# Kernel optimization log

Measured on AMD Instinct MI355X. Metric: run time of the kernel, lower is better.

Reference implementation:

```python
import jax, jax.numpy as jnp
import numpy as np

N_PTS = 2_000_000
N_VOX = 500_000
N_EMB = 1_000_000
EMBED_DIM = 16


def _interp_offset():
    # 8 corners of the unit cube, same order as torch.meshgrid([0,1]*3) -> reshape(-1,3)
    o = jnp.array([0.0, 1.0], dtype=jnp.float32)
    return jnp.stack(jnp.meshgrid(o, o, o, indexing='ij'), axis=-1).reshape(-1, 3)  # [8,3]


def setup_inputs() -> dict:
    key = jax.random.key(0)
    k1, k2, k3, k4, k5 = jax.random.split(key, 5)
    pts = jax.random.uniform(k1, (N_PTS, 3), dtype=jnp.float32)
    p2v_idx = jax.random.randint(k2, (N_PTS,), 0, N_VOX, dtype=jnp.int64 if jax.config.jax_enable_x64 else jnp.int32)
    embeddings = jax.random.normal(k3, (N_EMB, EMBED_DIM), dtype=jnp.float32) * (EMBED_DIM ** -0.5)
    center_points = jax.random.uniform(k4, (N_VOX, 3), dtype=jnp.float32)
    center2corner = jax.random.randint(k5, (N_VOX, 8), 0, N_EMB, dtype=jnp.int64 if jax.config.jax_enable_x64 else jnp.int32)
    voxel_size = jnp.ones((1,), dtype=jnp.float32)
    return {"pts": pts, "p2v_idx": p2v_idx, "embeddings": embeddings,
            "center_points": center_points, "center2corner": center2corner,
            "voxel_size": voxel_size}


def reference(pts, p2v_idx, embeddings, center_points, center2corner, voxel_size):
    offset = _interp_offset()                      # [8,3]
    cp = center_points[p2v_idx]                    # [N,3]   gather voxel centers
    cidx = center2corner[p2v_idx]                  # [N,8]   gather corner indices
    emb = embeddings[cidx]                         # [N,8,D] gather corner embeddings
    # relative position inside voxel, in [0,1]
    p = (pts - cp) / voxel_size + 0.5              # [N,3]
    p = p[:, None, :]                              # [N,1,3]
    # trilinear weights: prod over xyz of (p if corner==1 else 1-p)
    r = jnp.prod(p * offset + (1.0 - p) * (1.0 - offset), axis=-1)  # [N,8]
    return jnp.einsum('nc,ncd->nd', r, emb)        # [N,D]
```

## Files before the change

kernel.cpp:

```cpp
#include <hip/hip_runtime.h>


typedef float v4f __attribute__((ext_vector_type(4)));


__global__ void k_init_gbase(unsigned* __restrict__ gbase, int NB, unsigned CAP) {
    int i = blockIdx.x * blockDim.x + threadIdx.x;
    if (i < NB) gbase[i] = (unsigned)i * CAP;
}

__global__ __launch_bounds__(1024) void k_bucket(
    const int*   __restrict__ p2v,
    const float* __restrict__ pts,
    unsigned*    __restrict__ gbase,
    unsigned*    __restrict__ vA,
    v4f*         __restrict__ recA,
    int N, int NB)
{
    __shared__ unsigned cnt[512];
    __shared__ unsigned cur[512];
    const int tid = threadIdx.x;
    const int i0 = (blockIdx.x * 1024 + tid) * 8;

    for (int b = tid; b < NB; b += 1024) cnt[b] = 0u;
    __syncthreads();

    int vv[8];
    const bool full = (i0 + 7 < N);
    if (full) {
        const int4 a = *(const int4*)(p2v + i0);
        const int4 b4 = *(const int4*)(p2v + i0 + 4);
        vv[0]=a.x; vv[1]=a.y; vv[2]=a.z; vv[3]=a.w;
        vv[4]=b4.x; vv[5]=b4.y; vv[6]=b4.z; vv[7]=b4.w;
        #pragma unroll
        for (int k = 0; k < 8; ++k) atomicAdd(&cnt[vv[k] >> 11], 1u);
    } else {
        for (int k = 0; k < 8; ++k)
            if (i0 + k < N) { vv[k] = p2v[i0 + k]; atomicAdd(&cnt[vv[k] >> 11], 1u); }
    }
    __syncthreads();

    for (int b = tid; b < NB; b += 1024) {
        const unsigned c = cnt[b];
        cur[b] = c ? atomicAdd(&gbase[b], c) : 0u;
    }
    __syncthreads();

    if (full) {
        const v4f* p4 = (const v4f*)pts;
        const size_t fb = (size_t)3 * (size_t)(i0 >> 2);
        const v4f f0 = p4[fb], f1 = p4[fb+1], f2 = p4[fb+2];
        const v4f f3 = p4[fb+3], f4 = p4[fb+4], f5 = p4[fb+5];
        const float xs[8] = {f0.x, f0.w, f1.z, f2.y, f3.x, f3.w, f4.z, f5.y};
        const float ys[8] = {f0.y, f1.x, f1.w, f2.z, f3.y, f4.x, f4.w, f5.z};
        const float zs[8] = {f0.z, f1.y, f2.x, f2.w, f3.z, f4.y, f5.x, f5.w};
        #pragma unroll
        for (int k = 0; k < 8; ++k) {
            const unsigned pos = atomicAdd(&cur[vv[k] >> 11], 1u);
            v4f r; r.x = xs[k]; r.y = ys[k]; r.z = zs[k]; r.w = __int_as_float(i0 + k);
            recA[pos] = r;
            vA[pos] = (unsigned)vv[k];
        }
    } else {
        for (int k = 0; k < 8; ++k) {
            const int i = i0 + k;
            if (i >= N) break;
            const unsigned pos = atomicAdd(&cur[vv[k] >> 11], 1u);
            v4f r;
            r.x = pts[3*(size_t)i]; r.y = pts[3*(size_t)i+1]; r.z = pts[3*(size_t)i+2];
            r.w = __int_as_float(i);
            recA[pos] = r;
            vA[pos] = (unsigned)vv[k];
        }
    }
}

__global__ __launch_bounds__(256) void k_main_b(
    const unsigned* __restrict__ gbase,
    const unsigned* __restrict__ vA,
    const v4f*      __restrict__ recA,
    const float* __restrict__ emb,
    const float* __restrict__ cp,
    const int*   __restrict__ c2c,
    const float* __restrict__ vox,
    float*       __restrict__ out,
    int NB)
{
    const int bid = blockIdx.x;
    const int x   = bid & 7;
    const int t2  = bid >> 3;
    const int c   = t2 >> 8;
    const int j   = t2 & 255;
    const int b   = (c << 3) | x;
    if (b >= NB) return;

    const unsigned base = (unsigned)b << 14;
    const unsigned cntb = gbase[b] - base;
    const unsigned local = (unsigned)(j << 6) + (threadIdx.x >> 2);
    if (local >= cntb) return;

    const unsigned n = base + local;
    const int q = threadIdx.x & 3;

    const unsigned v = vA[n];
    const v4f r = recA[n];
    const int orig = __float_as_int(r.w);

    const int4* c4 = (const int4*)(c2c + 8 * (size_t)v);
    const int4 ci0 = c4[0];
    const int4 ci1 = c4[1];
    const int cidx[8] = {ci0.x, ci0.y, ci0.z, ci0.w, ci1.x, ci1.y, ci1.z, ci1.w};

    v4f e[8];
    #pragma unroll
    for (int cc = 0; cc < 8; ++cc) {
        e[cc] = *(const v4f*)(emb + 16 * (size_t)cidx[cc] + 4 * q);
    }

    const float inv_vs = 1.0f / vox[0];
    const float* cpp = cp + 3 * (size_t)v;
    const float px = (r.x - cpp[0]) * inv_vs + 0.5f;
    const float py = (r.y - cpp[1]) * inv_vs + 0.5f;
    const float pz = (r.z - cpp[2]) * inv_vs + 0.5f;
    const float wx[2] = {1.0f - px, px};
    const float wy[2] = {1.0f - py, py};
    const float wz[2] = {1.0f - pz, pz};

    v4f acc = (v4f)(0.0f);
    #pragma unroll
    for (int cc = 0; cc < 8; ++cc) {
        const float w = wx[(cc >> 2) & 1] * wy[(cc >> 1) & 1] * wz[cc & 1];
        acc.x = fmaf(w, e[cc].x, acc.x);
        acc.y = fmaf(w, e[cc].y, acc.y);
        acc.z = fmaf(w, e[cc].z, acc.z);
        acc.w = fmaf(w, e[cc].w, acc.w);
    }

    __builtin_nontemporal_store(acc, (v4f*)(out + 16 * (size_t)orig + 4 * q));
}


__global__ void k_zero(unsigned* __restrict__ hist, int n) {
    int i = blockIdx.x * blockDim.x + threadIdx.x;
    if (i < n) hist[i] = 0u;
}

__global__ __launch_bounds__(256) void k_hist_rank(const int* __restrict__ p2v,
                                                   unsigned* __restrict__ hist,
                                                   unsigned* __restrict__ rank, int N) {
    const int base = (blockIdx.x * blockDim.x + threadIdx.x) * 8;
    if (base + 7 < N) {
        const int4 a = *(const int4*)(p2v + base);
        const int4 b = *(const int4*)(p2v + base + 4);
        const unsigned r0 = atomicAdd(&hist[a.x], 1u);
        const unsigned r1 = atomicAdd(&hist[a.y], 1u);
        const unsigned r2 = atomicAdd(&hist[a.z], 1u);
        const unsigned r3 = atomicAdd(&hist[a.w], 1u);
        const unsigned r4 = atomicAdd(&hist[b.x], 1u);
        const unsigned r5 = atomicAdd(&hist[b.y], 1u);
        const unsigned r6 = atomicAdd(&hist[b.z], 1u);
        const unsigned r7 = atomicAdd(&hist[b.w], 1u);
        uint4 o0; o0.x = r0; o0.y = r1; o0.z = r2; o0.w = r3;
        uint4 o1; o1.x = r4; o1.y = r5; o1.z = r6; o1.w = r7;
        *(uint4*)(rank + base)     = o0;
        *(uint4*)(rank + base + 4) = o1;
    } else {
        for (int k = 0; k < 8; ++k)
            if (base + k < N) rank[base + k] = atomicAdd(&hist[p2v[base + k]], 1u);
    }
}

__global__ __launch_bounds__(256) void k_scan_blocks(unsigned* __restrict__ hist,
                                                     unsigned* __restrict__ bsums, int nbins) {
    __shared__ unsigned tsum[256];
    const int tid = threadIdx.x;
    const int i0 = blockIdx.x * 1024 + tid * 4;
    unsigned v[4]; unsigned s = 0;
    #pragma unroll
    for (int k = 0; k < 4; ++k) {
        unsigned c = (i0 + k < nbins) ? hist[i0 + k] : 0u;
        v[k] = s; s += c;
    }
    tsum[tid] = s; __syncthreads();
    for (int off = 1; off < 256; off <<= 1) {
        unsigned x = tsum[tid];
        unsigned y = (tid >= off) ? tsum[tid - off] : 0u;
        __syncthreads();
        tsum[tid] = x + y;
        __syncthreads();
    }
    unsigned prefix = (tid > 0) ? tsum[tid - 1] : 0u;
    #pragma unroll
    for (int k = 0; k < 4; ++k) {
        if (i0 + k < nbins) hist[i0 + k] = prefix + v[k];
    }
    if (tid == 255) bsums[blockIdx.x] = tsum[255];
}

__global__ __launch_bounds__(256) void k_scan_sums(unsigned* __restrict__ bsums, int nb) {
    __shared__ unsigned tsum[256];
    const int tid = threadIdx.x;
    const int i0 = tid * 4;
    unsigned v[4]; unsigned s = 0;
    #pragma unroll
    for (int k = 0; k < 4; ++k) {
        unsigned c = (i0 + k < nb) ? bsums[i0 + k] : 0u;
        v[k] = s; s += c;
    }
    tsum[tid] = s; __syncthreads();
    for (int off = 1; off < 256; off <<= 1) {
        unsigned x = tsum[tid];
        unsigned y = (tid >= off) ? tsum[tid - off] : 0u;
        __syncthreads();
        tsum[tid] = x + y;
        __syncthreads();
    }
    unsigned prefix = (tid > 0) ? tsum[tid - 1] : 0u;
    #pragma unroll
    for (int k = 0; k < 4; ++k) {
        if (i0 + k < nb) bsums[i0 + k] = prefix + v[k];
    }
}

__global__ __launch_bounds__(256) void k_place(
    const float* __restrict__ pts,
    const int*   __restrict__ p2v,
    const unsigned* __restrict__ rank,
    const unsigned* __restrict__ hist,
    const unsigned* __restrict__ bsums,
    unsigned* __restrict__ vsort,
    v4f*      __restrict__ rec,
    int N)
{
    const int base = (blockIdx.x * blockDim.x + threadIdx.x) * 4;
    if (base + 3 < N) {
        const int4  v4r = *(const int4*)(p2v + base);
        const uint4 r4  = *(const uint4*)(rank + base);
        const v4f* p4 = (const v4f*)pts;
        const size_t f0i = (size_t)(3 * (base >> 2));
        const v4f f0 = p4[f0i];
        const v4f f1 = p4[f0i + 1];
        const v4f f2 = p4[f0i + 2];

        const unsigned pos0 = hist[v4r.x] + bsums[((unsigned)v4r.x) >> 10] + r4.x;
        const unsigned pos1 = hist[v4r.y] + bsums[((unsigned)v4r.y) >> 10] + r4.y;
        const unsigned pos2 = hist[v4r.z] + bsums[((unsigned)v4r.z) >> 10] + r4.z;
        const unsigned pos3 = hist[v4r.w] + bsums[((unsigned)v4r.w) >> 10] + r4.w;

        vsort[pos0] = (unsigned)v4r.x;
        vsort[pos1] = (unsigned)v4r.y;
        vsort[pos2] = (unsigned)v4r.z;
        vsort[pos3] = (unsigned)v4r.w;

        v4f a;
        a.x = f0.x; a.y = f0.y; a.z = f0.z; a.w = __int_as_float(base + 0);
        rec[pos0] = a;
        a.x = f0.w; a.y = f1.x; a.z = f1.y; a.w = __int_as_float(base + 1);
        rec[pos1] = a;
        a.x = f1.z; a.y = f1.w; a.z = f2.x; a.w = __int_as_float(base + 2);
        rec[pos2] = a;
        a.x = f2.y; a.y = f2.z; a.z = f2.w; a.w = __int_as_float(base + 3);
        rec[pos3] = a;
    } else {
        for (int k = 0; k < 4; ++k) {
            const int i = base + k;
            if (i >= N) break;
            const int v = p2v[i];
            const unsigned pos = hist[v] + bsums[((unsigned)v) >> 10] + rank[i];
            vsort[pos] = (unsigned)v;
            v4f r;
            r.x = pts[3 * (size_t)i + 0];
            r.y = pts[3 * (size_t)i + 1];
            r.z = pts[3 * (size_t)i + 2];
            r.w = __int_as_float(i);
            rec[pos] = r;
        }
    }
}

__global__ __launch_bounds__(256) void k_main(
    const unsigned* __restrict__ vsort, const v4f* __restrict__ rec,
    const float* __restrict__ emb,
    const float* __restrict__ cp,
    const int*   __restrict__ c2c,
    const float* __restrict__ vox,
    float*       __restrict__ out,
    int n0, int n1)
{
    const int t = blockIdx.x * blockDim.x + threadIdx.x;
    const int n = n0 + (t >> 2);
    const int q = t & 3;
    if (n >= n1) return;

    const unsigned v = vsort[n];
    const v4f r = rec[n];
    const int orig = __float_as_int(r.w);

    const int4* c4 = (const int4*)(c2c + 8 * (size_t)v);
    const int4 ci0 = c4[0];
    const int4 ci1 = c4[1];
    const int cidx[8] = {ci0.x, ci0.y, ci0.z, ci0.w, ci1.x, ci1.y, ci1.z, ci1.w};

    v4f e[8];
    #pragma unroll
    for (int c = 0; c < 8; ++c) {
        e[c] = *(const v4f*)(emb + 16 * (size_t)cidx[c] + 4 * q);
    }

    const float inv_vs = 1.0f / vox[0];
    const float* cpp = cp + 3 * (size_t)v;
    const float px = (r.x - cpp[0]) * inv_vs + 0.5f;
    const float py = (r.y - cpp[1]) * inv_vs + 0.5f;
    const float pz = (r.z - cpp[2]) * inv_vs + 0.5f;
    const float wx[2] = {1.0f - px, px};
    const float wy[2] = {1.0f - py, py};
    const float wz[2] = {1.0f - pz, pz};

    v4f acc = (v4f)(0.0f);
    #pragma unroll
    for (int c = 0; c < 8; ++c) {
        const float w = wx[(c >> 2) & 1] * wy[(c >> 1) & 1] * wz[c & 1];
        acc.x = fmaf(w, e[c].x, acc.x);
        acc.y = fmaf(w, e[c].y, acc.y);
        acc.z = fmaf(w, e[c].z, acc.z);
        acc.w = fmaf(w, e[c].w, acc.w);
    }

    __builtin_nontemporal_store(acc, (v4f*)(out + 16 * (size_t)orig + 4 * q));
}

__global__ __launch_bounds__(256) void k_direct(
    const float* __restrict__ pts, const int* __restrict__ p2v,
    const float* __restrict__ emb, const float* __restrict__ cp,
    const int* __restrict__ c2c, const float* __restrict__ vox,
    float* __restrict__ out, int N)
{
    const int t = blockIdx.x * blockDim.x + threadIdx.x;
    const int n = t >> 2, q = t & 3;
    if (n >= N) return;
    const int v = p2v[n];
    const int4* c4 = (const int4*)(c2c + 8 * (size_t)v);
    const int4 ci0 = c4[0], ci1 = c4[1];
    const int cidx[8] = {ci0.x, ci0.y, ci0.z, ci0.w, ci1.x, ci1.y, ci1.z, ci1.w};
    v4f e[8];
    #pragma unroll
    for (int c = 0; c < 8; ++c) e[c] = *(const v4f*)(emb + 16 * (size_t)cidx[c] + 4 * q);
    const float inv_vs = 1.0f / vox[0];
    const float* pp = pts + 3 * (size_t)n;
    const float* cpp = cp + 3 * (size_t)v;
    const float px = (pp[0] - cpp[0]) * inv_vs + 0.5f;
    const float py = (pp[1] - cpp[1]) * inv_vs + 0.5f;
    const float pz = (pp[2] - cpp[2]) * inv_vs + 0.5f;
    const float wx[2] = {1.0f - px, px};
    const float wy[2] = {1.0f - py, py};
    const float wz[2] = {1.0f - pz, pz};
    v4f acc = (v4f)(0.0f);
    #pragma unroll
    for (int c = 0; c < 8; ++c) {
        const float w = wx[(c >> 2) & 1] * wy[(c >> 1) & 1] * wz[c & 1];
        acc.x = fmaf(w, e[c].x, acc.x); acc.y = fmaf(w, e[c].y, acc.y);
        acc.z = fmaf(w, e[c].z, acc.z); acc.w = fmaf(w, e[c].w, acc.w);
    }
    __builtin_nontemporal_store(acc, (v4f*)(out + 4 * (size_t)t));
}


extern "C" void kernel_launch(void* const* d_in, const int* in_sizes, int n_in,
                              void* d_out, int out_size, void* d_ws, size_t ws_size,
                              hipStream_t stream) {
    const float* pts = (const float*)d_in[0];
    const int*   p2v = (const int*)d_in[1];
    const float* emb = (const float*)d_in[2];
    const float* cp  = (const float*)d_in[3];
    const int*   c2c = (const int*)d_in[4];
    const float* vox = (const float*)d_in[5];
    float*       out = (float*)d_out;

    const int N  = in_sizes[1];
    const int NV = in_sizes[4] / 8;
    const int block = 256;

    const int NB = (NV + 2047) >> 11;
    const unsigned CAP = 16384u;
    if (NB >= 1 && NB <= 512 && (unsigned)(N / NB) + 2048u <= CAP) {
        const size_t off_gbase = 0;
        const size_t off_vA    = 8192;
        const size_t sz_vA     = (size_t)NB * CAP * 4u;
        const size_t off_recA  = (off_vA + sz_vA + 255u) & ~(size_t)255u;
        const size_t need_fast = off_recA + (size_t)NB * CAP * 16u;

        if (ws_size >= need_fast) {
            unsigned* gbase = (unsigned*)((char*)d_ws + off_gbase);
            unsigned* vA    = (unsigned*)((char*)d_ws + off_vA);
            v4f*      recA  = (v4f*)((char*)d_ws + off_recA);

            k_init_gbase<<<(NB + block - 1) / block, block, 0, stream>>>(gbase, NB, CAP);
            k_bucket<<<(N + 8191) / 8192, 1024, 0, stream>>>(p2v, pts, gbase, vA, recA, N, NB);

            const int classes = (NB + 7) >> 3;
            const int grid = 8 * classes * 256;
            k_main_b<<<grid, block, 0, stream>>>(
                gbase, vA, recA, emb, cp, c2c, vox, out, NB);
            return;
        }
    }

    {
        const size_t MB = 1024u * 1024u;
        const size_t off_hist  = 0;
        const size_t off_bsums = 2u * MB;
        const size_t off_rank  = 4u * MB;
        const size_t off_vsort = 12u * MB;
        const size_t off_rec   = 20u * MB;
        const size_t need = off_rec + (size_t)N * 16u;

        if (ws_size >= need) {
            unsigned* hist  = (unsigned*)((char*)d_ws + off_hist);
            unsigned* bsums = (unsigned*)((char*)d_ws + off_bsums);
            unsigned* rank  = (unsigned*)((char*)d_ws + off_rank);
            unsigned* vsort = (unsigned*)((char*)d_ws + off_vsort);
            v4f*      rec   = (v4f*)((char*)d_ws + off_rec);

            const int nscan = (NV + 1023) / 1024;

            k_zero<<<(NV + block - 1) / block, block, 0, stream>>>(hist, NV);
            k_hist_rank<<<(N + block * 8 - 1) / (block * 8), block, 0, stream>>>(p2v, hist, rank, N);
            k_scan_blocks<<<nscan, 256, 0, stream>>>(hist, bsums, NV);
            k_scan_sums<<<1, 256, 0, stream>>>(bsums, nscan);
            k_place<<<(N + block * 4 - 1) / (block * 4), block, 0, stream>>>(
                pts, p2v, rank, hist, bsums, vsort, rec, N);

            const long long threads = 4LL * N;
            k_main<<<(int)((threads + block - 1) / block), block, 0, stream>>>(
                vsort, rec, emb, cp, c2c, vox, out, 0, N);
            return;
        }
    }

    {
        const long long threads = 4LL * N;
        k_direct<<<(int)((threads + block - 1) / block), block, 0, stream>>>(
            pts, p2v, emb, cp, c2c, vox, out, N);
    }
}
```

Measured before the change: 388.8 us.

## Sort points by voxel within bucket segments in shared memory before gathering

The main kernel now splits each coarse bucket into segments of up to 4096 points, handled by 1024-thread blocks. Each block does a shared-memory counting sort by voxel id (histogram, scan, scatter of local indices). It then processes points in voxel order, so points in the same voxel read the same center, corner-index and embedding rows close together in time and get better cache reuse. The cost is extra passes over vA, block-wide barriers, large shared-memory use that limits occupancy, and far fewer blocks in the grid.

Measured after the change: 456.4 us. +17.4%, slower.

```diff
diff --git a/kernel.cpp b/kernel.cpp
--- a/kernel.cpp
+++ b/kernel.cpp
@@ -75,7 +75,7 @@
     }
 }
 
-__global__ __launch_bounds__(256) void k_main_b(
+__global__ __launch_bounds__(1024) void k_main_s(
     const unsigned* __restrict__ gbase,
     const unsigned* __restrict__ vA,
     const v4f*      __restrict__ recA,
@@ -86,57 +86,101 @@
     float*       __restrict__ out,
     int NB)
 {
+    __shared__ unsigned h[2048];
+    __shared__ unsigned tsum[1024];
+    __shared__ unsigned short ordl[4096];
+
     const int bid = blockIdx.x;
     const int x   = bid & 7;
     const int t2  = bid >> 3;
-    const int c   = t2 >> 8;
-    const int j   = t2 & 255;
+    const int c   = t2 >> 2;
+    const int s   = t2 & 3;
     const int b   = (c << 3) | x;
     if (b >= NB) return;
 
+    const int tid = threadIdx.x;
     const unsigned base = (unsigned)b << 14;
     const unsigned cntb = gbase[b] - base;
-    const unsigned local = (unsigned)(j << 6) + (threadIdx.x >> 2);
-    if (local >= cntb) return;
-
-    const unsigned n = base + local;
-    const int q = threadIdx.x & 3;
-
-    const unsigned v = vA[n];
-    const v4f r = recA[n];
-    const int orig = __float_as_int(r.w);
-
-    const int4* c4 = (const int4*)(c2c + 8 * (size_t)v);
-    const int4 ci0 = c4[0];
-    const int4 ci1 = c4[1];
-    const int cidx[8] = {ci0.x, ci0.y, ci0.z, ci0.w, ci1.x, ci1.y, ci1.z, ci1.w};
-
-    v4f e[8];
-    #pragma unroll
-    for (int cc = 0; cc < 8; ++cc) {
-        e[cc] = *(const v4f*)(emb + 16 * (size_t)cidx[cc] + 4 * q);
-    }
-
+    const int seg0 = s << 12;
+    const int segN = min((int)cntb - seg0, 4096);
+    if (segN <= 0) return;
+
+    const unsigned sbase = base + (unsigned)seg0;
+    const unsigned vbase = (unsigned)b << 11;
+
+    h[tid] = 0u; h[tid + 1024] = 0u;
+    __syncthreads();
+
+    for (int j = tid; j < segN; j += 1024)
+        atomicAdd(&h[vA[sbase + j] - vbase], 1u);
+    __syncthreads();
+
+    const unsigned a0 = h[2 * tid];
+    const unsigned a1 = h[2 * tid + 1];
+    tsum[tid] = a0 + a1; __syncthreads();
+    for (int off = 1; off < 1024; off <<= 1) {
+        unsigned xx = tsum[tid];
+        unsigned yy = (tid >= off) ? tsum[tid - off] : 0u;
+        __syncthreads();
+        tsum[tid] = xx + yy;
+        __syncthreads();
+    }
+    const unsigned pre = (tid > 0) ? tsum[tid - 1] : 0u;
+    h[2 * tid]     = pre;
+    h[2 * tid + 1] = pre + a0;
+    __syncthreads();
+
+    for (int j = tid; j < segN; j += 1024) {
+        const unsigned p = atomicAdd(&h[vA[sbase + j] - vbase], 1u);
+        ordl[p] = (unsigned short)j;
+    }
+    __syncthreads();
+
+    const int q = tid & 3;
+    const int pt = tid >> 2;
     const float inv_vs = 1.0f / vox[0];
-    const float* cpp = cp + 3 * (size_t)v;
-    const float px = (r.x - cpp[0]) * inv_vs + 0.5f;
-    const float py = (r.y - cpp[1]) * inv_vs + 0.5f;
-    const float pz = (r.z - cpp[2]) * inv_vs + 0.5f;
-    const float wx[2] = {1.0f - px, px};
-    const float wy[2] = {1.0f - py, py};
-    const float wz[2] = {1.0f - pz, pz};
-
-    v4f acc = (v4f)(0.0f);
-    #pragma unroll
-    for (int cc = 0; cc < 8; ++cc) {
-        const float w = wx[(cc >> 2) & 1] * wy[(cc >> 1) & 1] * wz[cc & 1];
-        acc.x = fmaf(w, e[cc].x, acc.x);
-        acc.y = fmaf(w, e[cc].y, acc.y);
-        acc.z = fmaf(w, e[cc].z, acc.z);
-        acc.w = fmaf(w, e[cc].w, acc.w);
-    }
-
-    __builtin_nontemporal_store(acc, (v4f*)(out + 16 * (size_t)orig + 4 * q));
+    const int npass = (segN + 255) >> 8;
+    for (int pass = 0; pass < npass; ++pass) {
+        const int p = (pass << 8) + pt;
+        if (p >= segN) break;
+        const int j = (int)ordl[p];
+        const unsigned n = sbase + (unsigned)j;
+
+        const unsigned v = vA[n];
+        const v4f r = recA[n];
+        const int orig = __float_as_int(r.w);
+
+        const int4* c4 = (const int4*)(c2c + 8 * (size_t)v);
+        const int4 ci0 = c4[0];
+        const int4 ci1 = c4[1];
+        const int cidx[8] = {ci0.x, ci0.y, ci0.z, ci0.w, ci1.x, ci1.y, ci1.z, ci1.w};
+
+        v4f e[8];
+        #pragma unroll
+        for (int cc = 0; cc < 8; ++cc) {
+            e[cc] = *(const v4f*)(emb + 16 * (size_t)cidx[cc] + 4 * q);
+        }
+
+        const float* cpp = cp + 3 * (size_t)v;
+        const float px = (r.x - cpp[0]) * inv_vs + 0.5f;
+        const float py = (r.y - cpp[1]) * inv_vs + 0.5f;
+        const float pz = (r.z - cpp[2]) * inv_vs + 0.5f;
+        const float wx[2] = {1.0f - px, px};
+        const float wy[2] = {1.0f - py, py};
+        const float wz[2] = {1.0f - pz, pz};
+
+        v4f acc = (v4f)(0.0f);
+        #pragma unroll
+        for (int cc = 0; cc < 8; ++cc) {
+            const float w = wx[(cc >> 2) & 1] * wy[(cc >> 1) & 1] * wz[cc & 1];
+            acc.x = fmaf(w, e[cc].x, acc.x);
+            acc.y = fmaf(w, e[cc].y, acc.y);
+            acc.z = fmaf(w, e[cc].z, acc.z);
+            acc.w = fmaf(w, e[cc].w, acc.w);
+        }
+
+        __builtin_nontemporal_store(acc, (v4f*)(out + 16 * (size_t)orig + 4 * q));
+    }
 }
 
 
@@ -398,8 +442,8 @@
             k_bucket<<<(N + 8191) / 8192, 1024, 0, stream>>>(p2v, pts, gbase, vA, recA, N, NB);
 
             const int classes = (NB + 7) >> 3;
-            const int grid = 8 * classes * 256;
-            k_main_b<<<grid, block, 0, stream>>>(
+            const int grid = classes * 4 * 8;
+            k_main_s<<<grid, 1024, 0, stream>>>(
                 gbase, vA, recA, emb, cp, c2c, vox, out, NB);
             return;
         }
```
